# Kernel optimization log

Hardware: AMD Instinct MI355X
Metric: run time of the kernel (lower is better)

## Reference

```python
import jax, jax.numpy as jnp
import numpy as np

HEADS = 16
HEAD_DIM = 64  # hidden_size 1024 / 16 heads
NUM_TOKENS = 4
IP_SCALE = 1.0
LN_EPS = 1e-5


def setup_inputs() -> dict:
    key = jax.random.key(0)
    ks = jax.random.split(key, 12)
    B, Lq, D, Dc = 8, 4096, 1024, 768
    Lenc = 77 + NUM_TOKENS
    s = lambda fan: 1.0 / np.sqrt(fan)
    return {
        "hidden_states": jax.random.normal(ks[0], (B, Lq, D), jnp.float32),
        "encoder_hidden_states": jax.random.normal(ks[1], (B, Lenc, Dc), jnp.float32),
        "Wq": jax.random.normal(ks[2], (D, D), jnp.float32) * s(D),
        "Wk": jax.random.normal(ks[3], (D, Dc), jnp.float32) * s(Dc),
        "Wv": jax.random.normal(ks[4], (D, Dc), jnp.float32) * s(Dc),
        "Wk_ip": jax.random.normal(ks[5], (D, Dc), jnp.float32) * s(Dc),
        "Wv_ip": jax.random.normal(ks[6], (D, Dc), jnp.float32) * s(Dc),
        "Wo": jax.random.normal(ks[7], (D, D), jnp.float32) * s(D),
        "bo": jnp.zeros((D,), jnp.float32),
        "ln_w": jnp.ones((Dc,), jnp.float32),
        "ln_b": jnp.zeros((Dc,), jnp.float32),
    }


def _layernorm(x, w, b):
    mu = jnp.mean(x, axis=-1, keepdims=True)
    var = jnp.var(x, axis=-1, keepdims=True)
    return (x - mu) * jax.lax.rsqrt(var + LN_EPS) * w + b


def _heads(x):
    B, L, D = x.shape
    return x.reshape(B, L, HEADS, HEAD_DIM)


def _attend(q, k, v):
    # q: [B,Lq,H,Dh], k/v: [B,Lk,H,Dh]
    scale = 1.0 / np.sqrt(HEAD_DIM)
    scores = jnp.einsum("bqhd,bkhd->bhqk", q, k) * scale
    probs = jax.nn.softmax(scores, axis=-1)
    return jnp.einsum("bhqk,bkhd->bqhd", probs, v)


def reference(hidden_states, encoder_hidden_states, Wq, Wk, Wv, Wk_ip, Wv_ip, Wo, bo, ln_w, ln_b):
    B, Lq, D = hidden_states.shape
    end_pos = encoder_hidden_states.shape[1] - NUM_TOKENS
    text = encoder_hidden_states[:, :end_pos, :]
    ip = encoder_hidden_states[:, end_pos:, :]
    text = _layernorm(text, ln_w, ln_b)  # attn.norm_cross

    q = _heads(hidden_states @ Wq.T)
    k = _heads(text @ Wk.T)
    v = _heads(text @ Wv.T)
    base = _attend(q, k, v)  # [B,Lq,H,Dh]

    ip_k = _heads(ip @ Wk_ip.T)
    ip_v = _heads(ip @ Wv_ip.T)
    ip_out = _attend(q, ip_k, ip_v)

    out = (base + IP_SCALE * ip_out).reshape(B, Lq, D)
    return out @ Wo.T + bo
```

## Files before the change

kernel.cpp:

```cpp
#include <hip/hip_runtime.h>
#include <hip/hip_bf16.h>
#include <stdint.h>


typedef __attribute__((ext_vector_type(8))) short short8;
typedef __attribute__((ext_vector_type(4))) float f32x4;
typedef __attribute__((ext_vector_type(8))) float float8_t;
typedef __attribute__((ext_vector_type(8))) __bf16 bf16x8;
typedef __attribute__((ext_vector_type(4))) __bf16 bf16x4;

__device__ __forceinline__ ushort f2b(float f) {
  __bf16 h = (__bf16)f;
  return __builtin_bit_cast(ushort, h);
}

__device__ __forceinline__ short8 pack2(float4 a, float4 b) {
  float8_t v;
  v[0] = a.x; v[1] = a.y; v[2] = a.z; v[3] = a.w;
  v[4] = b.x; v[5] = b.y; v[6] = b.z; v[7] = b.w;
  return __builtin_bit_cast(short8, __builtin_convertvector(v, bf16x8));
}

#define GLD16(gp, lp) \
  __builtin_amdgcn_global_load_lds((const __attribute__((address_space(1))) uint32_t*)(gp), \
                                   (__attribute__((address_space(3))) uint32_t*)(lp), 16, 0, 0)

#define FENCE_SCHED() __builtin_amdgcn_sched_barrier(0)

struct CvtArgs {
  const float* src[6];
  ushort* dst[6];
  int n4[6];
};

__global__ __launch_bounds__(256) void k_prep(CvtArgs a,
                                              const float* __restrict__ enc,
                                              const float* __restrict__ lnw,
                                              const float* __restrict__ lnb,
                                              ushort* __restrict__ xn) {
  int seg = blockIdx.y;
  if (seg < 6) {
    int i = blockIdx.x * blockDim.x + threadIdx.x;
    if (i >= a.n4[seg]) return;
    float4 v = reinterpret_cast<const float4*>(a.src[seg])[i];
    bf16x4 h;
    h[0] = (__bf16)v.x; h[1] = (__bf16)v.y; h[2] = (__bf16)v.z; h[3] = (__bf16)v.w;
    reinterpret_cast<ushort4*>(a.dst[seg])[i] = __builtin_bit_cast(ushort4, h);
    return;
  }
  if (blockIdx.x >= 768) return;
  const int Dc = 768;
  int tok = blockIdx.x % 96, b = blockIdx.x / 96, t = threadIdx.x;
  ushort* out = xn + ((size_t)b * 96 + tok) * Dc;
  bool padrow = (tok >= 84) || (tok >= 77 && tok < 80);
  if (padrow) { out[t] = 0; out[t + 256] = 0; out[t + 512] = 0; return; }
  const float* src = (tok < 77) ? enc + ((size_t)b * 81 + tok) * Dc
                                : enc + ((size_t)b * 81 + 77 + (tok - 80)) * Dc;
  float x0 = src[t], x1 = src[t + 256], x2 = src[t + 512];
  if (tok >= 80) { out[t] = f2b(x0); out[t + 256] = f2b(x1); out[t + 512] = f2b(x2); return; }
  float s = x0 + x1 + x2, q = x0 * x0 + x1 * x1 + x2 * x2;
  for (int m = 32; m; m >>= 1) { s += __shfl_xor(s, m, 64); q += __shfl_xor(q, m, 64); }
  __shared__ float rs[4], rq[4];
  int w = t >> 6;
  if ((t & 63) == 0) { rs[w] = s; rq[w] = q; }
  __syncthreads();
  s = rs[0] + rs[1] + rs[2] + rs[3];
  q = rq[0] + rq[1] + rq[2] + rq[3];
  float mean = s * (1.0f / 768.0f);
  float var = q * (1.0f / 768.0f) - mean * mean;
  float rstd = rsqrtf(var + 1e-5f);
  out[t]       = f2b((x0 - mean) * rstd * lnw[t]       + lnb[t]);
  out[t + 256] = f2b((x1 - mean) * rstd * lnw[t + 256] + lnb[t + 256]);
  out[t + 512] = f2b((x2 - mean) * rstd * lnw[t + 512] + lnb[t + 512]);
}

__global__ __launch_bounds__(256) void k_kv(const ushort* __restrict__ xn,
                                            const ushort* __restrict__ wk,
                                            const ushort* __restrict__ wkip,
                                            const ushort* __restrict__ wv,
                                            const ushort* __restrict__ wvip,
                                            ushort* __restrict__ kall,
                                            ushort* __restrict__ vtall) {
  int mode = blockIdx.z;
  const ushort* wb   = mode ? wv   : wk;
  const ushort* wipb = mode ? wvip : wkip;
  ushort* out        = mode ? vtall : kall;
  int n0 = blockIdx.x * 64, b = blockIdx.y;
  int t = threadIdx.x, w = t >> 6, l = t & 63, lo = l & 15, hi = l >> 4;
  __shared__ alignas(16) ushort Xs[96 * 32];
  __shared__ alignas(16) ushort Ws[64 * 32];
  __shared__ alignas(16) ushort Wip[64 * 32];
  f32x4 acc[6];
  f32x4 zf = {0.f, 0.f, 0.f, 0.f};
  for (int i = 0; i < 6; i++) acc[i] = zf;
  const ushort* xb = xn + (size_t)b * 96 * 768;
  for (int k0 = 0; k0 < 768; k0 += 32) {
    __syncthreads();
    for (int i = t; i < 96 * 16; i += 256) {
      int row = i >> 4, p = i & 15;
      reinterpret_cast<uint32_t*>(Xs)[i] =
          *reinterpret_cast<const uint32_t*>(xb + row * 768 + k0 + p * 2);
    }
    for (int i = t; i < 64 * 16; i += 256) {
      int row = i >> 4, p = i & 15;
      reinterpret_cast<uint32_t*>(Ws)[i] =
          *reinterpret_cast<const uint32_t*>(wb + (size_t)(n0 + row) * 768 + k0 + p * 2);
      reinterpret_cast<uint32_t*>(Wip)[i] =
          *reinterpret_cast<const uint32_t*>(wipb + (size_t)(n0 + row) * 768 + k0 + p * 2);
    }
    __syncthreads();
    short8 a[6], bb, bip;
    for (int mi = 0; mi < 6; mi++)
      a[mi] = *reinterpret_cast<const short8*>(Xs + (mi * 16 + lo) * 32 + hi * 8);
    bb  = *reinterpret_cast<const short8*>(Ws  + (w * 16 + lo) * 32 + hi * 8);
    bip = *reinterpret_cast<const short8*>(Wip + (w * 16 + lo) * 32 + hi * 8);
    for (int mi = 0; mi < 5; mi++)
      acc[mi] = __builtin_amdgcn_mfma_f32_16x16x32_bf16(a[mi], bb, acc[mi], 0, 0, 0);
    acc[5] = __builtin_amdgcn_mfma_f32_16x16x32_bf16(a[5], bip, acc[5], 0, 0, 0);
  }
  for (int mi = 0; mi < 6; mi++) {
    int col = n0 + w * 16 + lo;
    int h = col >> 6, dd = col & 63;
    for (int j = 0; j < 4; j++) {
      int tok = mi * 16 + hi * 4 + j;
      ushort v = f2b(acc[mi][j]);
      if (mode == 0) out[(((size_t)b * 16 + h) * 96 + tok) * 64 + dd] = v;
      else           out[(((size_t)b * 16 + h) * 64 + dd) * 96 + tok] = v;
    }
  }
}

__global__ __launch_bounds__(512, 2) void k_qg8(const float* __restrict__ A,
                                                const ushort* __restrict__ Bw,
                                                const ushort* __restrict__ Kall,
                                                const ushort* __restrict__ Vt,
                                                ushort* __restrict__ attnO) {
  const int K = 1024, NT = 16;
  int wg = blockIdx.x;
  int nid = (wg & 7) * 64 + (wg >> 3);
  int m0 = (nid >> 2) * 256, n0 = (nid & 3) * 256;
  int t = threadIdx.x, wid = t >> 6, l = t & 63, lo = l & 15, hi = l >> 4;
  int wr = wid >> 2, wc = wid & 3;
  __shared__ alignas(16) ushort SMEM[81920];
  ushort* ASb = SMEM;
  ushort* BSb = SMEM + 32768;
  f32x4 acc[8][4];
  f32x4 zf = {0.f, 0.f, 0.f, 0.f};
#pragma unroll
  for (int i = 0; i < 8; i++)
#pragma unroll
    for (int j = 0; j < 4; j++) acc[i][j] = zf;
  int tr = t >> 3, tc = t & 7;
  int tcs = tc ^ (tr & 7);
  const float*  gA = A  + (size_t)(m0 + tr) * K + tcs * 8;
  const ushort* gB = Bw + (size_t)(n0 + tr) * K + tcs * 8;
  float4 av[4][2];

#define LD_A(kt_) do { \
    _Pragma("unroll") \
    for (int s_ = 0; s_ < 4; s_++) { \
      av[s_][0] = *reinterpret_cast<const float4*>(gA + (size_t)s_ * 64 * K + (kt_) * 64); \
      av[s_][1] = *reinterpret_cast<const float4*>(gA + (size_t)s_ * 64 * K + (kt_) * 64 + 4); \
    } } while (0)
#define WR_A(s_, b_) \
    *reinterpret_cast<short8*>(&ASb[(b_) * 16384 + (s_) * 4096 + t * 8]) = pack2(av[s_][0], av[s_][1])
#define STG_B(kt_, s_, b_) GLD16(gB + (size_t)(s_) * 64 * K + (kt_) * 64, &BSb[(b_) * 16384 + (s_) * 4096 + wid * 512])

  LD_A(0);
  STG_B(0, 0, 0); STG_B(0, 1, 0); STG_B(0, 2, 0); STG_B(0, 3, 0);
  STG_B(1, 0, 1); STG_B(1, 1, 1); STG_B(1, 2, 1); STG_B(1, 3, 1);
  WR_A(0, 0); WR_A(1, 0); WR_A(2, 0); WR_A(3, 0);
  LD_A(1);
  WR_A(0, 1); WR_A(1, 1); WR_A(2, 1); WR_A(3, 1);
  asm volatile("s_waitcnt lgkmcnt(0)" ::: "memory");
  __builtin_amdgcn_s_barrier();
  FENCE_SCHED();

  const int swz = (lo & 7) << 3;
  short8 af[4][2], af2[4][2], b01[2][2], b23[2][2];

  for (int kt = 0; kt < NT; kt++) {
    int cur = kt & 1, nxt = cur ^ 1;
    const ushort* sA = &ASb[cur * 16384];
    const ushort* sB = &BSb[cur * 16384];
#pragma unroll
    for (int q = 0; q < 4; q++)
#pragma unroll
      for (int kk = 0; kk < 2; kk++)
        af[q][kk] = *reinterpret_cast<const short8*>(
            sA + (wr * 128 + q * 16 + lo) * 64 + ((hi * 8 + kk * 32) ^ swz));
#pragma unroll
    for (int n = 0; n < 2; n++)
#pragma unroll
      for (int kk = 0; kk < 2; kk++) {
        b01[n][kk] = *reinterpret_cast<const short8*>(
            sB + (wc * 64 + n * 16 + lo) * 64 + ((hi * 8 + kk * 32) ^ swz));
        b23[n][kk] = *reinterpret_cast<const short8*>(
            sB + (wc * 64 + (2 + n) * 16 + lo) * 64 + ((hi * 8 + kk * 32) ^ swz));
      }
    __builtin_amdgcn_s_barrier();
    FENCE_SCHED();
    __builtin_amdgcn_s_setprio(1);
#pragma unroll
    for (int q = 0; q < 4; q++)
#pragma unroll
      for (int n = 0; n < 2; n++)
#pragma unroll
        for (int kk = 0; kk < 2; kk++) {
          acc[q][n]     = __builtin_amdgcn_mfma_f32_16x16x32_bf16(af[q][kk], b01[n][kk], acc[q][n], 0, 0, 0);
          acc[q][2 + n] = __builtin_amdgcn_mfma_f32_16x16x32_bf16(af[q][kk], b23[n][kk], acc[q][2 + n], 0, 0, 0);
        }
    __builtin_amdgcn_s_setprio(0);
    __builtin_amdgcn_s_barrier();
    FENCE_SCHED();
#pragma unroll
    for (int q = 0; q < 4; q++)
#pragma unroll
      for (int kk = 0; kk < 2; kk++)
        af2[q][kk] = *reinterpret_cast<const short8*>(
            sA + (wr * 128 + (4 + q) * 16 + lo) * 64 + ((hi * 8 + kk * 32) ^ swz));
    if (kt + 2 < NT) { STG_B(kt + 2, 0, cur); STG_B(kt + 2, 1, cur); }
    if (kt + 1 < NT) { WR_A(0, nxt); WR_A(1, nxt); }
    __builtin_amdgcn_s_barrier();
    FENCE_SCHED();
    __builtin_amdgcn_s_setprio(1);
#pragma unroll
    for (int q = 0; q < 4; q++)
#pragma unroll
      for (int n = 0; n < 2; n++)
#pragma unroll
        for (int kk = 0; kk < 2; kk++)
          acc[4 + q][2 + n] = __builtin_amdgcn_mfma_f32_16x16x32_bf16(af2[q][kk], b23[n][kk], acc[4 + q][2 + n], 0, 0, 0);
    __builtin_amdgcn_s_setprio(0);
    __builtin_amdgcn_s_barrier();
    FENCE_SCHED();
    if (kt + 2 < NT) { STG_B(kt + 2, 2, cur); STG_B(kt + 2, 3, cur); }
    if (kt + 1 < NT) { WR_A(2, nxt); WR_A(3, nxt); }
    asm volatile("s_waitcnt vmcnt(4)" ::: "memory");
    asm volatile("s_waitcnt lgkmcnt(0)" ::: "memory");
    if (kt + 2 < NT) LD_A(kt + 2);
    __builtin_amdgcn_s_barrier();
    FENCE_SCHED();
    __builtin_amdgcn_s_setprio(1);
#pragma unroll
    for (int q = 0; q < 4; q++)
#pragma unroll
      for (int n = 0; n < 2; n++)
#pragma unroll
        for (int kk = 0; kk < 2; kk++)
          acc[4 + q][n] = __builtin_amdgcn_mfma_f32_16x16x32_bf16(af2[q][kk], b01[n][kk], acc[4 + q][n], 0, 0, 0);
    __builtin_amdgcn_s_setprio(0);
    __builtin_amdgcn_s_barrier();
    FENCE_SCHED();
  }
#undef LD_A
#undef WR_A
#undef STG_B

  __syncthreads();
  ushort* ep = SMEM + wid * 8192;
#pragma unroll
  for (int mi = 0; mi < 8; mi++)
#pragma unroll
    for (int n = 0; n < 4; n++)
#pragma unroll
      for (int j = 0; j < 4; j++) {
        int row_l = mi * 16 + hi * 4 + j;
        int col = n * 16 + lo;
        ep[row_l * 64 + (((col >> 3) ^ (row_l & 7)) << 3) + (col & 7)] = f2b(acc[mi][n][j]);
      }
  ushort* PS = SMEM + 65536 + wid * 2048;
  int b = m0 >> 12;
  int h = (n0 >> 6) + wc;
  const ushort* Kb = Kall + (size_t)(b * 16 + h) * 96 * 64;
  const ushort* Vb = Vt + (size_t)(b * 16 + h) * 64 * 96;
  short8 kf[6][2], vf[3][4];
#pragma unroll
  for (int ni = 0; ni < 6; ni++)
#pragma unroll
    for (int ks = 0; ks < 2; ks++)
      kf[ni][ks] = *reinterpret_cast<const short8*>(Kb + (ni * 16 + lo) * 64 + ks * 32 + hi * 8);
#pragma unroll
  for (int kk = 0; kk < 3; kk++)
#pragma unroll
    for (int dn = 0; dn < 4; dn++)
      vf[kk][dn] = *reinterpret_cast<const short8*>(Vb + (dn * 16 + lo) * 96 + kk * 32 + hi * 8);
  const float SC = 0.125f * 1.44269504088896340736f;

  short8 qf[2];
  f32x4 s[6];
#define QK_LOAD(mi_) do { \
    _Pragma("unroll") \
    for (int ks = 0; ks < 2; ks++) \
      qf[ks] = *reinterpret_cast<const short8*>( \
          &ep[((mi_) * 16 + lo) * 64 + (((ks * 4 + hi) ^ (lo & 7)) << 3)]); \
  } while (0)
#define QK_MFMA() do { \
    _Pragma("unroll") \
    for (int ni = 0; ni < 6; ni++) { \
      s[ni] = zf; \
      _Pragma("unroll") \
      for (int ks = 0; ks < 2; ks++) \
        s[ni] = __builtin_amdgcn_mfma_f32_16x16x32_bf16(qf[ks], kf[ni][ks], s[ni], 0, 0, 0); \
    } } while (0)

  QK_LOAD(0); QK_MFMA();
  for (int mi = 0; mi < 8; mi++) {
    float rb4[4];
#pragma unroll
    for (int j = 0; j < 4; j++) {
      float pb[5];
      float sb = 0.f;
#pragma unroll
      for (int ni = 0; ni < 5; ni++) {
        int c = ni * 16 + lo;
        float p = (c < 77) ? exp2f(s[ni][j] * SC) : 0.f;
        pb[ni] = p; sb += p;
      }
      sb += __shfl_xor(sb, 1, 64); sb += __shfl_xor(sb, 2, 64);
      sb += __shfl_xor(sb, 4, 64); sb += __shfl_xor(sb, 8, 64);
      rb4[j] = __builtin_amdgcn_rcpf(sb);
      bool val = lo < 4;
      float pi = val ? exp2f(s[5][j] * SC) : 0.f;
      float si = pi;
      si += __shfl_xor(si, 1, 64); si += __shfl_xor(si, 2, 64);
      ushort* pr = &PS[(hi * 4 + j) * 104];
#pragma unroll
      for (int ni = 0; ni < 5; ni++) pr[ni * 16 + lo] = f2b(pb[ni]);
      pr[80 + lo] = f2b(val ? pi * (sb * __builtin_amdgcn_rcpf(si)) : 0.f);
    }
    if (mi < 7) { QK_LOAD(mi + 1); QK_MFMA(); }
    f32x4 o[4];
#pragma unroll
    for (int dn = 0; dn < 4; dn++) o[dn] = zf;
#pragma unroll
    for (int kk = 0; kk < 3; kk++) {
      short8 pf = *reinterpret_cast<const short8*>(&PS[lo * 104 + kk * 32 + hi * 8]);
#pragma unroll
      for (int dn = 0; dn < 4; dn++)
        o[dn] = __builtin_amdgcn_mfma_f32_16x16x32_bf16(pf, vf[kk][dn], o[dn], 0, 0, 0);
    }
#pragma unroll
    for (int dn = 0; dn < 4; dn++)
#pragma unroll
      for (int j = 0; j < 4; j++) {
        int row_l = hi * 4 + j;
        int col = dn * 16 + lo;
        PS[row_l * 64 + (((col >> 3) ^ (row_l & 7)) << 3) + (col & 7)] = f2b(o[dn][j] * rb4[j]);
      }
    int gr0 = m0 + wr * 128 + mi * 16;
#pragma unroll
    for (int it = 0; it < 2; it++) {
      int row_o = it * 8 + (l >> 3), c8 = l & 7;
      short8 v = *reinterpret_cast<const short8*>(
          &PS[row_o * 64 + ((c8 ^ (row_o & 7)) << 3)]);
      *reinterpret_cast<short8*>(&attnO[(size_t)(gr0 + row_o) * 1024 + h * 64 + c8 * 8]) = v;
    }
  }
#undef QK_LOAD
#undef QK_MFMA
}

__global__ __launch_bounds__(512, 2) void k_og8(const ushort* __restrict__ A,
                                                const ushort* __restrict__ Bw,
                                                const float* __restrict__ bias,
                                                float* __restrict__ C) {
  const int K = 1024, NT = 16;
  int wg = blockIdx.x;
  int nid = (wg & 7) * 64 + (wg >> 3);
  int m0 = (nid >> 2) * 256, n0 = (nid & 3) * 256;
  int t = threadIdx.x, wid = t >> 6, l = t & 63, lo = l & 15, hi = l >> 4;
  int wr = wid >> 2, wc = wid & 3;
  __shared__ alignas(16) ushort AS[2][256 * 64];
  __shared__ alignas(16) ushort BS[2][256 * 64];
  f32x4 acc[8][4];
  f32x4 zf = {0.f, 0.f, 0.f, 0.f};
#pragma unroll
  for (int i = 0; i < 8; i++)
#pragma unroll
    for (int j = 0; j < 4; j++) acc[i][j] = zf;
  int tr = t >> 3, tc = t & 7;
  int tcs = tc ^ (tr & 7);
  const ushort* gA = A  + (size_t)(m0 + tr) * K + tcs * 8;
  const ushort* gB = Bw + (size_t)(n0 + tr) * K + tcs * 8;

#define STG_A(kt_, s_, b_) GLD16(gA + (size_t)(s_) * 64 * K + (kt_) * 64, &AS[b_][(s_) * 4096 + wid * 512])
#define STG_B(kt_, s_, b_) GLD16(gB + (size_t)(s_) * 64 * K + (kt_) * 64, &BS[b_][(s_) * 4096 + wid * 512])

  STG_A(0, 0, 0); STG_A(0, 1, 0); STG_A(0, 2, 0); STG_A(0, 3, 0);
  STG_B(0, 0, 0); STG_B(0, 1, 0); STG_B(0, 2, 0); STG_B(0, 3, 0);
  STG_B(1, 0, 1); STG_B(1, 1, 1); STG_B(1, 2, 1); STG_B(1, 3, 1);
  STG_A(1, 0, 1); STG_A(1, 1, 1);
  asm volatile("s_waitcnt vmcnt(6)" ::: "memory");
  __builtin_amdgcn_s_barrier();
  FENCE_SCHED();

  const int swz = (lo & 7) << 3;
  short8 af[4][2], af2[4][2], b01[2][2], b23[2][2];

  for (int kt = 0; kt < NT; kt++) {
    int cur = kt & 1, nxt = cur ^ 1;
    const ushort* sA = &AS[cur][0];
    const ushort* sB = &BS[cur][0];
#pragma unroll
    for (int q = 0; q < 4; q++)
#pragma unroll
      for (int kk = 0; kk < 2; kk++)
        af[q][kk] = *reinterpret_cast<const short8*>(
            sA + (wr * 128 + q * 16 + lo) * 64 + ((hi * 8 + kk * 32) ^ swz));
#pragma unroll
    for (int n = 0; n < 2; n++)
#pragma unroll
      for (int kk = 0; kk < 2; kk++) {
        b01[n][kk] = *reinterpret_cast<const short8*>(
            sB + (wc * 64 + n * 16 + lo) * 64 + ((hi * 8 + kk * 32) ^ swz));
        b23[n][kk] = *reinterpret_cast<const short8*>(
            sB + (wc * 64 + (2 + n) * 16 + lo) * 64 + ((hi * 8 + kk * 32) ^ swz));
      }
    if (kt + 1 < NT) { STG_A(kt + 1, 2, nxt); STG_A(kt + 1, 3, nxt); }
    __builtin_amdgcn_s_barrier();
    FENCE_SCHED();
    __builtin_amdgcn_s_setprio(1);
#pragma unroll
    for (int q = 0; q < 4; q++)
#pragma unroll
      for (int n = 0; n < 2; n++)
#pragma unroll
        for (int kk = 0; kk < 2; kk++) {
          acc[q][n]     = __builtin_amdgcn_mfma_f32_16x16x32_bf16(af[q][kk], b01[n][kk], acc[q][n], 0, 0, 0);
          acc[q][2 + n] = __builtin_amdgcn_mfma_f32_16x16x32_bf16(af[q][kk], b23[n][kk], acc[q][2 + n], 0, 0, 0);
        }
    __builtin_amdgcn_s_setprio(0);
    __builtin_amdgcn_s_barrier();
    FENCE_SCHED();
#pragma unroll
    for (int q = 0; q < 4; q++)
#pragma unroll
      for (int kk = 0; kk < 2; kk++)
        af2[q][kk] = *reinterpret_cast<const short8*>(
            sA + (wr * 128 + (4 + q) * 16 + lo) * 64 + ((hi * 8 + kk * 32) ^ swz));
    if (kt + 2 < NT) { STG_B(kt + 2, 0, cur); STG_B(kt + 2, 1, cur); }
    __builtin_amdgcn_s_barrier();
    FENCE_SCHED();
    __builtin_amdgcn_s_setprio(1);
#pragma unroll
    for (int q = 0; q < 4; q++)
#pragma unroll
      for (int n = 0; n < 2; n++)
#pragma unroll
        for (int kk = 0; kk < 2; kk++)
          acc[4 + q][2 + n] = __builtin_amdgcn_mfma_f32_16x16x32_bf16(af2[q][kk], b23[n][kk], acc[4 + q][2 + n], 0, 0, 0);
    __builtin_amdgcn_s_setprio(0);
    __builtin_amdgcn_s_barrier();
    FENCE_SCHED();
    if (kt + 2 < NT) {
      STG_B(kt + 2, 2, cur); STG_B(kt + 2, 3, cur);
      STG_A(kt + 2, 0, cur); STG_A(kt + 2, 1, cur);
      asm volatile("s_waitcnt vmcnt(6)" ::: "memory");
    } else {
      asm volatile("s_waitcnt vmcnt(0)" ::: "memory");
    }
    __builtin_amdgcn_s_barrier();
    FENCE_SCHED();
    __builtin_amdgcn_s_setprio(1);
#pragma unroll
    for (int q = 0; q < 4; q++)
#pragma unroll
      for (int n = 0; n < 2; n++)
#pragma unroll
        for (int kk = 0; kk < 2; kk++)
          acc[4 + q][n] = __builtin_amdgcn_mfma_f32_16x16x32_bf16(af2[q][kk], b01[n][kk], acc[4 + q][n], 0, 0, 0);
    __builtin_amdgcn_s_setprio(0);
    __builtin_amdgcn_s_barrier();
    FENCE_SCHED();
  }
#pragma unroll
  for (int n = 0; n < 4; n++) {
    int c = n0 + wc * 64 + n * 16 + lo;
    float bv = bias[c];
#pragma unroll
    for (int mi = 0; mi < 8; mi++)
#pragma unroll
      for (int j = 0; j < 4; j++) {
        int r = m0 + wr * 128 + mi * 16 + hi * 4 + j;
        C[(size_t)r * 1024 + c] = acc[mi][n][j] + bv;
      }
  }
#undef STG_A
#undef STG_B
}

extern "C" void kernel_launch(void* const* d_in, const int* in_sizes, int n_in,
                              void* d_out, int out_size, void* d_ws, size_t ws_size,
                              hipStream_t stream) {
  const float* hs   = (const float*)d_in[0];
  const float* enc  = (const float*)d_in[1];
  const float* Wq   = (const float*)d_in[2];
  const float* Wk   = (const float*)d_in[3];
  const float* Wv   = (const float*)d_in[4];
  const float* Wkip = (const float*)d_in[5];
  const float* Wvip = (const float*)d_in[6];
  const float* Wo   = (const float*)d_in[7];
  const float* bo   = (const float*)d_in[8];
  const float* lnw  = (const float*)d_in[9];
  const float* lnb  = (const float*)d_in[10];
  float* out = (float*)d_out;

  ushort* p = (ushort*)d_ws;
  ushort* attn    = p; p += (size_t)32768 * 1024;
  ushort* wq_bf   = p; p += (size_t)1024 * 1024;
  ushort* wo_bf   = p; p += (size_t)1024 * 1024;
  ushort* wk_bf   = p; p += (size_t)1024 * 768;
  ushort* wkip_bf = p; p += (size_t)1024 * 768;
  ushort* wv_bf   = p; p += (size_t)1024 * 768;
  ushort* wvip_bf = p; p += (size_t)1024 * 768;
  ushort* xn      = p; p += (size_t)8 * 96 * 768;
  ushort* kall    = p; p += (size_t)8 * 16 * 96 * 64;
  ushort* vtall   = p; p += (size_t)8 * 16 * 96 * 64;

  CvtArgs ca;
  ca.src[0] = Wq;   ca.dst[0] = wq_bf;   ca.n4[0] = 262144;
  ca.src[1] = Wo;   ca.dst[1] = wo_bf;   ca.n4[1] = 262144;
  ca.src[2] = Wk;   ca.dst[2] = wk_bf;   ca.n4[2] = 196608;
  ca.src[3] = Wkip; ca.dst[3] = wkip_bf; ca.n4[3] = 196608;
  ca.src[4] = Wv;   ca.dst[4] = wv_bf;   ca.n4[4] = 196608;
  ca.src[5] = Wvip; ca.dst[5] = wvip_bf; ca.n4[5] = 196608;
  k_prep<<<dim3(1024, 7), 256, 0, stream>>>(ca, enc, lnw, lnb, xn);
  k_kv<<<dim3(16, 8, 2), 256, 0, stream>>>(xn, wk_bf, wkip_bf, wv_bf, wvip_bf, kall, vtall);
  k_qg8<<<512, 512, 0, stream>>>(hs, wq_bf, kall, vtall, attn);
  k_og8<<<512, 512, 0, stream>>>(attn, wo_bf, bo, out);
}
```

Before: 288.9 us.

## Pre-convert hidden states to bf16 and stream A tiles via async global-to-LDS loads

The prep kernel gains an extra segment that converts the fp32 hidden_states to bf16, using the unused second half of the output buffer as scratch. The Q-projection GEMM then loads its A operand with direct global-to-LDS loads, like the B operand. This replaces the register-staged fp32 loads and in-register bf16 packing, and the pipeline's wait counts are reorganised to match. The aim is fewer VGPRs, fewer LDS writes from registers, and half-width A reads in the GEMM, which reads each A tile once per column block. The cost is an extra full pass over the 128MB activation tensor, plus a 64MB write, before the GEMM.

Result: no change. 289.6 us (median of 2 runs) (+0.2%).

```diff
diff --git a/kernel.cpp b/kernel.cpp
--- a/kernel.cpp
+++ b/kernel.cpp
@@ -14,13 +14,6 @@
   return __builtin_bit_cast(ushort, h);
 }
 
-__device__ __forceinline__ short8 pack2(float4 a, float4 b) {
-  float8_t v;
-  v[0] = a.x; v[1] = a.y; v[2] = a.z; v[3] = a.w;
-  v[4] = b.x; v[5] = b.y; v[6] = b.z; v[7] = b.w;
-  return __builtin_bit_cast(short8, __builtin_convertvector(v, bf16x8));
-}
-
 #define GLD16(gp, lp) \
   __builtin_amdgcn_global_load_lds((const __attribute__((address_space(1))) uint32_t*)(gp), \
                                    (__attribute__((address_space(3))) uint32_t*)(lp), 16, 0, 0)
@@ -37,7 +30,9 @@
                                               const float* __restrict__ enc,
                                               const float* __restrict__ lnw,
                                               const float* __restrict__ lnb,
-                                              ushort* __restrict__ xn) {
+                                              ushort* __restrict__ xn,
+                                              const float* __restrict__ hs,
+                                              ushort* __restrict__ hs_bf) {
   int seg = blockIdx.y;
   if (seg < 6) {
     int i = blockIdx.x * blockDim.x + threadIdx.x;
@@ -46,6 +41,16 @@
     bf16x4 h;
     h[0] = (__bf16)v.x; h[1] = (__bf16)v.y; h[2] = (__bf16)v.z; h[3] = (__bf16)v.w;
     reinterpret_cast<ushort4*>(a.dst[seg])[i] = __builtin_bit_cast(ushort4, h);
+    return;
+  }
+  if (seg == 7) {
+    const int n4 = 8388608;
+    for (int i = blockIdx.x * 256 + threadIdx.x; i < n4; i += 1024 * 256) {
+      float4 v = reinterpret_cast<const float4*>(hs)[i];
+      bf16x4 h;
+      h[0] = (__bf16)v.x; h[1] = (__bf16)v.y; h[2] = (__bf16)v.z; h[3] = (__bf16)v.w;
+      reinterpret_cast<ushort4*>(hs_bf)[i] = __builtin_bit_cast(ushort4, h);
+    }
     return;
   }
   if (blockIdx.x >= 768) return;
@@ -130,7 +135,7 @@
   }
 }
 
-__global__ __launch_bounds__(512, 2) void k_qg8(const float* __restrict__ A,
+__global__ __launch_bounds__(512, 2) void k_qg8(const ushort* __restrict__ A,
                                                 const ushort* __restrict__ Bw,
                                                 const ushort* __restrict__ Kall,
                                                 const ushort* __restrict__ Vt,
@@ -152,27 +157,17 @@
     for (int j = 0; j < 4; j++) acc[i][j] = zf;
   int tr = t >> 3, tc = t & 7;
   int tcs = tc ^ (tr & 7);
-  const float*  gA = A  + (size_t)(m0 + tr) * K + tcs * 8;
+  const ushort* gA = A  + (size_t)(m0 + tr) * K + tcs * 8;
   const ushort* gB = Bw + (size_t)(n0 + tr) * K + tcs * 8;
-  float4 av[4][2];
-
-#define LD_A(kt_) do { \
-    _Pragma("unroll") \
-    for (int s_ = 0; s_ < 4; s_++) { \
-      av[s_][0] = *reinterpret_cast<const float4*>(gA + (size_t)s_ * 64 * K + (kt_) * 64); \
-      av[s_][1] = *reinterpret_cast<const float4*>(gA + (size_t)s_ * 64 * K + (kt_) * 64 + 4); \
-    } } while (0)
-#define WR_A(s_, b_) \
-    *reinterpret_cast<short8*>(&ASb[(b_) * 16384 + (s_) * 4096 + t * 8]) = pack2(av[s_][0], av[s_][1])
+
+#define STG_A(kt_, s_, b_) GLD16(gA + (size_t)(s_) * 64 * K + (kt_) * 64, &ASb[(b_) * 16384 + (s_) * 4096 + wid * 512])
 #define STG_B(kt_, s_, b_) GLD16(gB + (size_t)(s_) * 64 * K + (kt_) * 64, &BSb[(b_) * 16384 + (s_) * 4096 + wid * 512])
 
-  LD_A(0);
+  STG_A(0, 0, 0); STG_A(0, 1, 0); STG_A(0, 2, 0); STG_A(0, 3, 0);
   STG_B(0, 0, 0); STG_B(0, 1, 0); STG_B(0, 2, 0); STG_B(0, 3, 0);
   STG_B(1, 0, 1); STG_B(1, 1, 1); STG_B(1, 2, 1); STG_B(1, 3, 1);
-  WR_A(0, 0); WR_A(1, 0); WR_A(2, 0); WR_A(3, 0);
-  LD_A(1);
-  WR_A(0, 1); WR_A(1, 1); WR_A(2, 1); WR_A(3, 1);
-  asm volatile("s_waitcnt lgkmcnt(0)" ::: "memory");
+  STG_A(1, 0, 1); STG_A(1, 1, 1);
+  asm volatile("s_waitcnt vmcnt(6)" ::: "memory");
   __builtin_amdgcn_s_barrier();
   FENCE_SCHED();
 
@@ -198,6 +193,7 @@
         b23[n][kk] = *reinterpret_cast<const short8*>(
             sB + (wc * 64 + (2 + n) * 16 + lo) * 64 + ((hi * 8 + kk * 32) ^ swz));
       }
+    if (kt + 1 < NT) { STG_A(kt + 1, 2, nxt); STG_A(kt + 1, 3, nxt); }
     __builtin_amdgcn_s_barrier();
     FENCE_SCHED();
     __builtin_amdgcn_s_setprio(1);
@@ -220,7 +216,6 @@
         af2[q][kk] = *reinterpret_cast<const short8*>(
             sA + (wr * 128 + (4 + q) * 16 + lo) * 64 + ((hi * 8 + kk * 32) ^ swz));
     if (kt + 2 < NT) { STG_B(kt + 2, 0, cur); STG_B(kt + 2, 1, cur); }
-    if (kt + 1 < NT) { WR_A(0, nxt); WR_A(1, nxt); }
     __builtin_amdgcn_s_barrier();
     FENCE_SCHED();
     __builtin_amdgcn_s_setprio(1);
@@ -234,11 +229,13 @@
     __builtin_amdgcn_s_setprio(0);
     __builtin_amdgcn_s_barrier();
     FENCE_SCHED();
-    if (kt + 2 < NT) { STG_B(kt + 2, 2, cur); STG_B(kt + 2, 3, cur); }
-    if (kt + 1 < NT) { WR_A(2, nxt); WR_A(3, nxt); }
-    asm volatile("s_waitcnt vmcnt(4)" ::: "memory");
-    asm volatile("s_waitcnt lgkmcnt(0)" ::: "memory");
-    if (kt + 2 < NT) LD_A(kt + 2);
+    if (kt + 2 < NT) {
+      STG_B(kt + 2, 2, cur); STG_B(kt + 2, 3, cur);
+      STG_A(kt + 2, 0, cur); STG_A(kt + 2, 1, cur);
+      asm volatile("s_waitcnt vmcnt(6)" ::: "memory");
+    } else {
+      asm volatile("s_waitcnt vmcnt(0)" ::: "memory");
+    }
     __builtin_amdgcn_s_barrier();
     FENCE_SCHED();
     __builtin_amdgcn_s_setprio(1);
@@ -253,8 +250,7 @@
     __builtin_amdgcn_s_barrier();
     FENCE_SCHED();
   }
-#undef LD_A
-#undef WR_A
+#undef STG_A
 #undef STG_B
 
   __syncthreads();
@@ -505,6 +501,7 @@
   const float* lnw  = (const float*)d_in[9];
   const float* lnb  = (const float*)d_in[10];
   float* out = (float*)d_out;
+  ushort* hs_bf = (ushort*)d_out + (size_t)32768 * 1024;
 
   ushort* p = (ushort*)d_ws;
   ushort* attn    = p; p += (size_t)32768 * 1024;
@@ -525,8 +522,8 @@
   ca.src[3] = Wkip; ca.dst[3] = wkip_bf; ca.n4[3] = 196608;
   ca.src[4] = Wv;   ca.dst[4] = wv_bf;   ca.n4[4] = 196608;
   ca.src[5] = Wvip; ca.dst[5] = wvip_bf; ca.n4[5] = 196608;
-  k_prep<<<dim3(1024, 7), 256, 0, stream>>>(ca, enc, lnw, lnb, xn);
+  k_prep<<<dim3(1024, 8), 256, 0, stream>>>(ca, enc, lnw, lnb, xn, hs, hs_bf);
   k_kv<<<dim3(16, 8, 2), 256, 0, stream>>>(xn, wk_bf, wkip_bf, wv_bf, wvip_bf, kall, vtall);
-  k_qg8<<<512, 512, 0, stream>>>(hs, wq_bf, kall, vtall, attn);
+  k_qg8<<<512, 512, 0, stream>>>(hs_bf, wq_bf, kall, vtall, attn);
   k_og8<<<512, 512, 0, stream>>>(attn, wo_bf, bo, out);
 }
```
